# Optimization experiments

Hardware: AMD Instinct MI355X
Metric: run time of the kernel (lower is better)

## Reference

```python
import jax, jax.numpy as jnp
import numpy as np

B, T, C, N = 4, 1024, 960, 64
H = C // N
R_W, R_A, R_V, R_G = 64, 64, 32, 128
LN_EPS = 0.00064


def setup_inputs() -> dict:
    key = jax.random.key(0)
    ks = jax.random.split(key, 28)
    s = 0.5 / np.sqrt(C)
    u = lambda k, sh, sc: jax.random.uniform(k, sh, jnp.float32, -sc, sc)
    n = lambda k, sh, sc: jax.random.normal(k, sh, jnp.float32) * sc
    return {
        "x": jax.random.normal(ks[0], (B, T, C), jnp.float32),
        "v_first": jax.random.normal(ks[1], (B, T, C), jnp.float32),
        "x_r": jax.random.uniform(ks[2], (1, 1, C), jnp.float32),
        "x_w": jax.random.uniform(ks[3], (1, 1, C), jnp.float32),
        "x_k": jax.random.uniform(ks[4], (1, 1, C), jnp.float32),
        "x_v": jax.random.uniform(ks[5], (1, 1, C), jnp.float32),
        "x_a": jax.random.uniform(ks[6], (1, 1, C), jnp.float32),
        "x_g": jax.random.uniform(ks[7], (1, 1, C), jnp.float32),
        "w0": n(ks[8], (1, 1, C), 0.5) - 2.0,
        "w1": n(ks[9], (C, R_W), 0.02),
        "w2": n(ks[10], (R_W, C), 0.02),
        "a0": n(ks[11], (1, 1, C), 0.3),
        "a1": n(ks[12], (C, R_A), 0.02),
        "a2": n(ks[13], (R_A, C), 0.02),
        "v0": n(ks[14], (1, 1, C), 0.3) + 0.73,
        "v1": n(ks[15], (C, R_V), 0.02),
        "v2": n(ks[16], (R_V, C), 0.02),
        "g1": n(ks[17], (C, R_G), 0.02),
        "g2": n(ks[18], (R_G, C), 0.02),
        "k_k": n(ks[19], (1, 1, C), 0.1) + 0.71,
        "k_a": n(ks[20], (1, 1, C), 0.1) + 1.02,
        "r_k": n(ks[21], (H, N), 0.1) - 0.04,
        "Wr": u(ks[22], (C, C), s),
        "Wk": u(ks[23], (C, C), 0.1 * s),
        "Wv": u(ks[24], (C, C), s),
        "Wo": u(ks[25], (C, C), s),
        "ln_g": jnp.ones((C,), jnp.float32),
        "ln_b": jnp.zeros((C,), jnp.float32),
    }


def reference(x, v_first, x_r, x_w, x_k, x_v, x_a, x_g, w0, w1, w2,
              a0, a1, a2, v0, v1, v2, g1, g2, k_k, k_a, r_k,
              Wr, Wk, Wv, Wo, ln_g, ln_b):
    Bx, Tx, Cx = x.shape
    # token shift: xx[t] = x[t-1] - x[t], with x[-1] = 0
    xx = jnp.concatenate([jnp.zeros_like(x[:, :1]), x[:, :-1]], axis=1) - x
    xr = x + xx * x_r; xw = x + xx * x_w; xk = x + xx * x_k
    xv = x + xx * x_v; xa = x + xx * x_a; xg = x + xx * x_g
    r = xr @ Wr
    w_raw = w0 + jnp.tanh(xw @ w1) @ w2       # log-space decay
    k = xk @ Wk
    v = xv @ Wv
    # layer_id > 0: residual mix with layer-0 value
    v = v + (v_first - v) * jax.nn.sigmoid(v0 + (xv @ v1) @ v2)
    a = jax.nn.sigmoid(a0 + (xa @ a1) @ a2)   # in-context learning rate
    g = jax.nn.sigmoid(xg @ g1) @ g2          # gate
    kk = (k * k_k).reshape(Bx, Tx, H, N)
    kk = kk / jnp.maximum(jnp.linalg.norm(kk, axis=-1, keepdims=True), 1e-12)
    k = k * (1.0 + (a - 1.0) * k_a)
    f32 = jnp.float32
    rh = r.reshape(Bx, Tx, H, N).astype(f32)
    kh = k.reshape(Bx, Tx, H, N).astype(f32)
    vh = v.reshape(Bx, Tx, H, N).astype(f32)
    wh = jnp.exp(-jax.nn.softplus(-w_raw.reshape(Bx, Tx, H, N).astype(f32)) - 0.5)
    ah = (-kk).astype(f32)                              # removal key
    bh = (kk * a.reshape(Bx, Tx, H, N)).astype(f32)     # replacement key

    def step(state, inp):
        r_t, w_t, k_t, v_t, a_t, b_t = inp  # each (B,H,N); state (B,H,N,N)
        sa = jnp.einsum('bhij,bhj->bhi', state, a_t)
        state = (state * w_t[:, :, None, :]
                 + sa[..., None] * b_t[:, :, None, :]
                 + v_t[..., None] * k_t[:, :, None, :])
        out_t = jnp.einsum('bhij,bhj->bhi', state, r_t)
        return state, out_t

    tm = lambda u: jnp.transpose(u, (1, 0, 2, 3))  # time-major
    state0 = jnp.zeros((Bx, H, N, N), f32)
    _, wkv = jax.lax.scan(step, state0, (tm(rh), tm(wh), tm(kh), tm(vh), tm(ah), tm(bh)))
    wkv = jnp.transpose(wkv, (1, 0, 2, 3))  # (B,T,H,N)
    # GroupNorm with H groups == per-head layernorm over N
    mu = wkv.mean(-1, keepdims=True)
    var = wkv.var(-1, keepdims=True)
    xn = (wkv - mu) / jnp.sqrt(var + LN_EPS)
    xn = xn * ln_g.reshape(H, N) + ln_b.reshape(H, N)
    bonus = (rh * kh * r_k).sum(-1, keepdims=True) * vh  # r*k*v bonus term
    xo = (xn + bonus).astype(x.dtype).reshape(Bx, Tx, Cx)
    return (xo * g) @ Wo


if __name__ == "__main__":
    out = reference(**setup_inputs())
    print(out.shape, out.dtype)
```

## Files before the change

kernel.cpp:

```cpp
#include <hip/hip_runtime.h>
#include <hip/hip_bf16.h>
#include <math.h>

#define Tn 1024
#define Cn 960
#define Hn 15
#define Nn 64
#define Mn 4096

typedef short bf16x8 __attribute__((ext_vector_type(8)));
typedef float f32x4 __attribute__((ext_vector_type(4)));

#define MCc ((size_t)Mn * Cn)

__device__ __forceinline__ float sigmf(float x) { return 1.0f / (1.0f + __expf(-x)); }

__device__ __forceinline__ ushort f2bf(float x) {
    unsigned u = __float_as_uint(x);
    unsigned r = (u + 0x7FFFu + ((u >> 16) & 1u)) >> 16;
    return (ushort)r;
}
__device__ __forceinline__ float bf2f(ushort h) { return __uint_as_float(((unsigned)h) << 16); }

__device__ __forceinline__ float rowsum16(float x) {
    x += __int_as_float(__builtin_amdgcn_update_dpp(0, __float_as_int(x), 0x121, 0xF, 0xF, true));
    x += __int_as_float(__builtin_amdgcn_update_dpp(0, __float_as_int(x), 0x122, 0xF, 0xF, true));
    x += __int_as_float(__builtin_amdgcn_update_dpp(0, __float_as_int(x), 0x124, 0xF, 0xF, true));
    x += __int_as_float(__builtin_amdgcn_update_dpp(0, __float_as_int(x), 0x128, 0xF, 0xF, true));
    return x;
}

__global__ __launch_bounds__(256) void mix6_kernel(
    const float* __restrict__ x,
    const float* __restrict__ mr, const float* __restrict__ mw, const float* __restrict__ mk,
    const float* __restrict__ mv, const float* __restrict__ ma, const float* __restrict__ mg,
    ushort* __restrict__ r_sp, ushort* __restrict__ w_sp, ushort* __restrict__ k_sp,
    ushort* __restrict__ v_sp, ushort* __restrict__ a_sp, ushort* __restrict__ g_sp)
{
    int idx = blockIdx.x * 256 + threadIdx.x;
    int e = idx * 4;
    if (e >= Mn * Cn) return;
    int m = e / Cn;
    int c = e - m * Cn;
    int t = m & (Tn - 1);
    float4 xv = *(const float4*)(x + e);
    float4 xp = make_float4(0.f, 0.f, 0.f, 0.f);
    if (t > 0) xp = *(const float4*)(x + e - Cn);
    float4 dx = make_float4(xp.x - xv.x, xp.y - xv.y, xp.z - xv.z, xp.w - xv.w);
#define MIXSPLIT(MIXP, P)                                                     \
    {                                                                         \
        float4 mm = *(const float4*)(MIXP + c);                               \
        float4 O = make_float4(xv.x + dx.x * mm.x, xv.y + dx.y * mm.y,        \
                               xv.z + dx.z * mm.z, xv.w + dx.w * mm.w);       \
        ushort h0 = f2bf(O.x), h1 = f2bf(O.y), h2 = f2bf(O.z), h3 = f2bf(O.w);\
        ushort l0 = f2bf(O.x - bf2f(h0)), l1 = f2bf(O.y - bf2f(h1));          \
        ushort l2 = f2bf(O.z - bf2f(h2)), l3 = f2bf(O.w - bf2f(h3));          \
        *(ushort4*)(P + e) = make_ushort4(h0, h1, h2, h3);                    \
        *(ushort4*)(P + MCc + e) = make_ushort4(l0, l1, l2, l3);              \
    }
    MIXSPLIT(mr, r_sp)
    MIXSPLIT(mw, w_sp)
    MIXSPLIT(mk, k_sp)
    MIXSPLIT(mv, v_sp)
    MIXSPLIT(ma, a_sp)
    MIXSPLIT(mg, g_sp)
#undef MIXSPLIT
}

__global__ __launch_bounds__(256) void convWT_kernel(
    const float* __restrict__ W, ushort* __restrict__ Thi, ushort* __restrict__ Tlo)
{
    __shared__ float tile[32][33];
    int k0 = blockIdx.x * 32, n0 = blockIdx.y * 32;
    int tx = threadIdx.x & 31, ty = threadIdx.x >> 5;
#pragma unroll
    for (int i = 0; i < 4; ++i)
        tile[ty + 8 * i][tx] = W[(size_t)(k0 + ty + 8 * i) * 960 + n0 + tx];
    __syncthreads();
#pragma unroll
    for (int i = 0; i < 4; ++i) {
        float x = tile[tx][ty + 8 * i];
        ushort h = f2bf(x);
        ushort l = f2bf(x - bf2f(h));
        size_t o = (size_t)(n0 + ty + 8 * i) * 960 + k0 + tx;
        Thi[o] = h;
        Tlo[o] = l;
    }
}

__global__ __launch_bounds__(256) void wprep_kernel(
    const float* __restrict__ w1, const float* __restrict__ a1,
    const float* __restrict__ v1, const float* __restrict__ g1,
    const float* __restrict__ w2, const float* __restrict__ a2,
    const float* __restrict__ v2, const float* __restrict__ g2,
    ushort* __restrict__ arena)
{
    __shared__ float tile[32][33];
    int z = blockIdx.z;
    const float* src;
    int K, N;
    size_t off;
    switch (z) {
        case 0: src = w1; K = 960; N = 64;  off = 0;      break;
        case 1: src = a1; K = 960; N = 64;  off = 122880; break;
        case 2: src = v1; K = 960; N = 32;  off = 245760; break;
        case 3: src = g1; K = 960; N = 128; off = 307200; break;
        case 4: src = w2; K = 64;  N = 960; off = 552960; break;
        case 5: src = a2; K = 64;  N = 960; off = 675840; break;
        case 6: src = v2; K = 32;  N = 960; off = 798720; break;
        default: src = g2; K = 128; N = 960; off = 860160; break;
    }
    int k0 = blockIdx.x * 32, n0 = blockIdx.y * 32;
    if (k0 >= K || n0 >= N) return;
    int tx = threadIdx.x & 31, ty = threadIdx.x >> 5;
#pragma unroll
    for (int i = 0; i < 4; ++i)
        tile[ty + 8 * i][tx] = src[(size_t)(k0 + ty + 8 * i) * N + n0 + tx];
    __syncthreads();
    ushort* Thi = arena + off;
    ushort* Tlo = arena + off + (size_t)K * N;
#pragma unroll
    for (int i = 0; i < 4; ++i) {
        float x = tile[tx][ty + 8 * i];
        ushort h = f2bf(x);
        ushort l = f2bf(x - bf2f(h));
        size_t o = (size_t)(n0 + ty + 8 * i) * K + k0 + tx;
        Thi[o] = h;
        Tlo[o] = l;
    }
}

__global__ __launch_bounds__(256) void convN_kernel(
    const float* __restrict__ X, ushort* __restrict__ hi, ushort* __restrict__ lo, int n4)
{
    int idx = blockIdx.x * 256 + threadIdx.x;
    if (idx >= n4) return;
    int e = idx * 4;
    float4 x = *(const float4*)(X + e);
    ushort h0 = f2bf(x.x), h1 = f2bf(x.y), h2 = f2bf(x.z), h3 = f2bf(x.w);
    ushort l0 = f2bf(x.x - bf2f(h0)), l1 = f2bf(x.y - bf2f(h1));
    ushort l2 = f2bf(x.z - bf2f(h2)), l3 = f2bf(x.w - bf2f(h3));
    *(ushort4*)(hi + e) = make_ushort4(h0, h1, h2, h3);
    *(ushort4*)(lo + e) = make_ushort4(l0, l1, l2, l3);
}

__global__ __launch_bounds__(512) void gemm_bf3_kernel(
    const ushort* __restrict__ Ahi, const ushort* __restrict__ Alo,
    const ushort* __restrict__ Bhi, const ushort* __restrict__ Blo,
    float* __restrict__ C, int ldc)
{
    __shared__ __align__(16) ushort sA[2][2][128][40];
    __shared__ __align__(16) ushort sB[2][2][64][40];
    const int K = 960;
    int bm = blockIdx.x * 128, bn = blockIdx.y * 64;
    int t = threadIdx.x;
    int w = t >> 6, l = t & 63;
    int lr = l & 15, lk = l >> 4;

    int ar = t >> 2, aseg = t & 3;
    int brr = t >> 2;
    int bhl = brr >> 6, brow = brr & 63, bseg = t & 3;
    const ushort* gAh = Ahi + (size_t)(bm + ar) * K + aseg * 8;
    const ushort* gAl = Alo + (size_t)(bm + ar) * K + aseg * 8;
    const ushort* gB = (bhl ? Blo : Bhi) + (size_t)(bn + brow) * K + bseg * 8;

    f32x4 acc[4];
#pragma unroll
    for (int j = 0; j < 4; ++j)
#pragma unroll
        for (int e = 0; e < 4; ++e) acc[j][e] = 0.f;

    float4 rhP, rlP, rbP, rhQ, rlQ, rbQ;
#define LOADP(KOFF)                                                           \
    {                                                                         \
        rhP = *(const float4*)(gAh + (KOFF));                                 \
        rlP = *(const float4*)(gAl + (KOFF));                                 \
        rbP = *(const float4*)(gB + (KOFF));                                  \
    }
#define LOADQ(KOFF)                                                           \
    {                                                                         \
        rhQ = *(const float4*)(gAh + (KOFF));                                 \
        rlQ = *(const float4*)(gAl + (KOFF));                                 \
        rbQ = *(const float4*)(gB + (KOFF));                                  \
    }
#define WRITEP(BUF)                                                           \
    {                                                                         \
        *(float4*)&sA[BUF][0][ar][aseg * 8] = rhP;                            \
        *(float4*)&sA[BUF][1][ar][aseg * 8] = rlP;                            \
        *(float4*)&sB[BUF][bhl][brow][bseg * 8] = rbP;                        \
    }
#define WRITEQ(BUF)                                                           \
    {                                                                         \
        *(float4*)&sA[BUF][0][ar][aseg * 8] = rhQ;                            \
        *(float4*)&sA[BUF][1][ar][aseg * 8] = rlQ;                            \
        *(float4*)&sB[BUF][bhl][brow][bseg * 8] = rbQ;                        \
    }
#define COMPUTEK(BUF)                                                         \
    {                                                                         \
        bf16x8 ah, al, bh[4], bl[4];                                          \
        ah = *(const bf16x8*)&sA[BUF][0][16 * w + lr][lk * 8];                \
        al = *(const bf16x8*)&sA[BUF][1][16 * w + lr][lk * 8];                \
        _Pragma("unroll")                                                     \
        for (int j = 0; j < 4; ++j) {                                         \
            bh[j] = *(const bf16x8*)&sB[BUF][0][16 * j + lr][lk * 8];         \
            bl[j] = *(const bf16x8*)&sB[BUF][1][16 * j + lr][lk * 8];         \
        }                                                                     \
        _Pragma("unroll")                                                     \
        for (int j = 0; j < 4; ++j) {                                         \
            acc[j] = __builtin_amdgcn_mfma_f32_16x16x32_bf16(ah, bh[j], acc[j], 0, 0, 0); \
            acc[j] = __builtin_amdgcn_mfma_f32_16x16x32_bf16(ah, bl[j], acc[j], 0, 0, 0); \
            acc[j] = __builtin_amdgcn_mfma_f32_16x16x32_bf16(al, bh[j], acc[j], 0, 0, 0); \
        }                                                                     \
    }

    LOADP(0)
    WRITEP(0)
    LOADQ(32)
    asm volatile("s_waitcnt lgkmcnt(0)" ::: "memory");
    __builtin_amdgcn_s_barrier();

    int cur = 0;
    for (int ks = 0; ks < 30; ks += 2) {
        int k2 = (ks + 2 < 30 ? ks + 2 : 29) * 32;
        LOADP(k2)
        COMPUTEK(cur)
        WRITEQ(cur ^ 1)
        asm volatile("s_waitcnt lgkmcnt(0)" ::: "memory");
        __builtin_amdgcn_s_barrier();
        cur ^= 1;
        int k3 = (ks + 3 < 30 ? ks + 3 : 29) * 32;
        LOADQ(k3)
        COMPUTEK(cur)
        WRITEP(cur ^ 1)
        asm volatile("s_waitcnt lgkmcnt(0)" ::: "memory");
        __builtin_amdgcn_s_barrier();
        cur ^= 1;
    }

#pragma unroll
    for (int j = 0; j < 4; ++j)
#pragma unroll
        for (int jr = 0; jr < 4; ++jr) {
            int row = bm + 16 * w + lk * 4 + jr;
            int col = bn + 16 * j + lr;
            C[(size_t)row * ldc + col] = acc[j][jr];
        }
#undef COMPUTEK
#undef WRITEP
#undef WRITEQ
#undef LOADP
#undef LOADQ
}

__device__ __forceinline__ void lora_core(
    const ushort* __restrict__ Ahi, const ushort* __restrict__ Alo, int lda,
    const ushort* __restrict__ Bhi, const ushort* __restrict__ Blo,
    float* __restrict__ C, int ldc, int Nvalid, int K, int act, int bn)
{
    __shared__ __align__(16) ushort sA[2][2][128][40];
    __shared__ __align__(16) ushort sB[2][2][64][40];
    int bm = blockIdx.x * 128;
    int t = threadIdx.x;
    int w = t >> 6, l = t & 63;
    int lr = l & 15, lk = l >> 4;

    int ar = t >> 2, aseg = t & 3;
    int brr = t >> 2;
    int bhl = brr >> 6, brow = brr & 63, bseg = t & 3;
    const ushort* gAh = Ahi + (size_t)(bm + ar) * lda + aseg * 8;
    const ushort* gAl = Alo + (size_t)(bm + ar) * lda + aseg * 8;
    const ushort* gB = (bhl ? Blo : Bhi) + (size_t)(bn + brow) * K + bseg * 8;

    f32x4 acc[4];
#pragma unroll
    for (int j = 0; j < 4; ++j)
#pragma unroll
        for (int e = 0; e < 4; ++e) acc[j][e] = 0.f;

    float4 rhP, rlP, rbP, rhQ, rlQ, rbQ;
#define LLOADP(KOFF)                                                          \
    {                                                                         \
        rhP = *(const float4*)(gAh + (KOFF));                                 \
        rlP = *(const float4*)(gAl + (KOFF));                                 \
        rbP = *(const float4*)(gB + (KOFF));                                  \
    }
#define LLOADQ(KOFF)                                                          \
    {                                                                         \
        rhQ = *(const float4*)(gAh + (KOFF));                                 \
        rlQ = *(const float4*)(gAl + (KOFF));                                 \
        rbQ = *(const float4*)(gB + (KOFF));                                  \
    }
#define LWRITEP(BUF)                                                          \
    {                                                                         \
        *(float4*)&sA[BUF][0][ar][aseg * 8] = rhP;                            \
        *(float4*)&sA[BUF][1][ar][aseg * 8] = rlP;                            \
        *(float4*)&sB[BUF][bhl][brow][bseg * 8] = rbP;                        \
    }
#define LWRITEQ(BUF)                                                          \
    {                                                                         \
        *(float4*)&sA[BUF][0][ar][aseg * 8] = rhQ;                            \
        *(float4*)&sA[BUF][1][ar][aseg * 8] = rlQ;                            \
        *(float4*)&sB[BUF][bhl][brow][bseg * 8] = rbQ;                        \
    }
#define LCOMPUTE(BUF)                                                         \
    {                                                                         \
        bf16x8 ah, al, bh[4], bl[4];                                          \
        ah = *(const bf16x8*)&sA[BUF][0][16 * w + lr][lk * 8];                \
        al = *(const bf16x8*)&sA[BUF][1][16 * w + lr][lk * 8];                \
        _Pragma("unroll")                                                     \
        for (int j = 0; j < 4; ++j) {                                         \
            bh[j] = *(const bf16x8*)&sB[BUF][0][16 * j + lr][lk * 8];         \
            bl[j] = *(const bf16x8*)&sB[BUF][1][16 * j + lr][lk * 8];         \
        }                                                                     \
        _Pragma("unroll")                                                     \
        for (int j = 0; j < 4; ++j) {                                         \
            acc[j] = __builtin_amdgcn_mfma_f32_16x16x32_bf16(ah, bh[j], acc[j], 0, 0, 0); \
            acc[j] = __builtin_amdgcn_mfma_f32_16x16x32_bf16(ah, bl[j], acc[j], 0, 0, 0); \
            acc[j] = __builtin_amdgcn_mfma_f32_16x16x32_bf16(al, bh[j], acc[j], 0, 0, 0); \
        }                                                                     \
    }

    int nk = K >> 5;
    LLOADP(0)
    LWRITEP(0)
    if (nk > 1) LLOADQ(32)
    asm volatile("s_waitcnt lgkmcnt(0)" ::: "memory");
    __builtin_amdgcn_s_barrier();

    int cur = 0;
    for (int ks = 0; ks < nk; ++ks) {
        int k2 = (ks + 2 < nk ? ks + 2 : nk - 1) * 32;
        if (!(ks & 1)) { LLOADP(k2) } else { LLOADQ(k2) }
        LCOMPUTE(cur)
        if (ks + 1 < nk) {
            if (!(ks & 1)) { LWRITEQ(cur ^ 1) } else { LWRITEP(cur ^ 1) }
            asm volatile("s_waitcnt lgkmcnt(0)" ::: "memory");
            __builtin_amdgcn_s_barrier();
        }
        cur ^= 1;
    }

#pragma unroll
    for (int j = 0; j < 4; ++j)
#pragma unroll
        for (int jr = 0; jr < 4; ++jr) {
            int row = bm + 16 * w + lk * 4 + jr;
            int col = bn + 16 * j + lr;
            if (col < Nvalid) {
                float v = acc[j][jr];
                if (act == 1) v = tanhf(v);
                else if (act == 2) v = sigmf(v);
                C[(size_t)row * ldc + col] = v;
            }
        }
#undef LCOMPUTE
#undef LWRITEP
#undef LWRITEQ
#undef LLOADP
#undef LLOADQ
}

__global__ __launch_bounds__(512) void lora_down_kernel(
    const ushort* __restrict__ xw_sp, const ushort* __restrict__ xa_sp,
    const ushort* __restrict__ xv_sp, const ushort* __restrict__ xg_sp,
    const ushort* __restrict__ arena, float* __restrict__ hid)
{
    int z = blockIdx.z;
    int bn = blockIdx.y * 64;
    const ushort* A;
    size_t off;
    int N, act, coff;
    switch (z) {
        case 0: A = xw_sp; off = 0;      N = 64;  act = 1; coff = 0;   break;
        case 1: A = xa_sp; off = 122880; N = 64;  act = 0; coff = 64;  break;
        case 2: A = xv_sp; off = 245760; N = 32;  act = 0; coff = 128; break;
        default: A = xg_sp; off = 307200; N = 128; act = 2; coff = 160; break;
    }
    if (bn >= N) return;
    lora_core(A, A + MCc, Cn, arena + off, arena + off + (size_t)960 * N,
              hid + coff, 288, N, 960, act, bn);
}

__global__ __launch_bounds__(512) void lora_up_kernel(
    const ushort* __restrict__ hidHi, const ushort* __restrict__ hidLo,
    const ushort* __restrict__ arena,
    float* __restrict__ oW, float* __restrict__ oA,
    float* __restrict__ oV, float* __restrict__ oG)
{
    int z = blockIdx.z;
    int bn = blockIdx.y * 64;
    size_t off;
    int K, aoff;
    float* C;
    switch (z) {
        case 0: off = 552960; K = 64;  aoff = 0;   C = oW; break;
        case 1: off = 675840; K = 64;  aoff = 64;  C = oA; break;
        case 2: off = 798720; K = 32;  aoff = 128; C = oV; break;
        default: off = 860160; K = 128; aoff = 160; C = oG; break;
    }
    lora_core(hidHi + aoff, hidLo + aoff, 288, arena + off,
              arena + off + (size_t)K * 960, C, Cn, Cn, K, 0, bn);
}

__global__ __launch_bounds__(256, 2) void scan_kernel(
    const float* __restrict__ rP, const float* __restrict__ wrawP,
    const float* __restrict__ apreP, const float* __restrict__ vsigP,
    const float* __restrict__ krawP, const float* __restrict__ vrawP,
    const float* __restrict__ vfirstP, const float* __restrict__ gP,
    const float* __restrict__ w0, const float* __restrict__ a0,
    const float* __restrict__ v0c, const float* __restrict__ kkc,
    const float* __restrict__ kac, const float* __restrict__ r_k,
    const float* __restrict__ ln_g, const float* __restrict__ ln_b,
    ushort* __restrict__ xsp)
{
    __shared__ float buf[2][7][16][64];
    __shared__ float outL[16][64];
    int tid = threadIdx.x;
    int q = tid >> 6, l = tid & 63;
    int blk = blockIdx.x;
    int bh = blk >> 3, seg = blk & 7;
    int bb = bh / Hn, h = bh - bb * Hn;
    size_t base = (size_t)bb * Tn * Cn + h * 64;
    int rg = l >> 4, cg = l & 15;
    int row0 = 16 * q + 4 * rg;
    int c0 = 4 * cg;

    int sstep = tid >> 4, sseg = tid & 15;
    size_t soff = base + (size_t)sstep * Cn + sseg * 4;
    int wofs = sstep * 64 + sseg * 4;
    int ccol = h * 64 + sseg * 4;

    int cbeg = (seg == 0) ? 0 : 8 * seg - 4;
    int cendc = 8 * seg + 8;
    int coutc = 8 * seg;

    float4 w0c4 = *(const float4*)(w0 + ccol);
    float4 a0c4 = *(const float4*)(a0 + ccol);
    float4 v0c4 = *(const float4*)(v0c + ccol);
    float4 kkc4 = *(const float4*)(kkc + ccol);
    float4 kac4 = *(const float4*)(kac + ccol);
    float4 rk4 = *(const float4*)(r_k + ccol);
    float4 lg4 = *(const float4*)(ln_g + ccol);
    float4 lb4 = *(const float4*)(ln_b + ccol);

    float s[4][4];
#pragma unroll
    for (int r = 0; r < 4; ++r)
#pragma unroll
        for (int c = 0; c < 4; ++c) s[r][c] = 0.f;

    float4 g_r, g_wr, g_vr, g_vf, g_vs, g_g, g_kr, g_ap;

#define LOADSTAGE(OFF)                                                        \
    g_r = *(const float4*)(rP + soff + (OFF));                                \
    g_wr = *(const float4*)(wrawP + soff + (OFF));                            \
    g_vr = *(const float4*)(vrawP + soff + (OFF));                            \
    g_vf = *(const float4*)(vfirstP + soff + (OFF));                          \
    g_vs = *(const float4*)(vsigP + soff + (OFF));                            \
    g_g = *(const float4*)(gP + soff + (OFF));                                \
    g_kr = *(const float4*)(krawP + soff + (OFF));                            \
    g_ap = *(const float4*)(apreP + soff + (OFF));

#define PARK(BN)                                                              \
    {                                                                         \
        const float E = 0.60653065971263342f;                                 \
        float4 w4;                                                            \
        w4.x = sigmf(w0c4.x + g_wr.x) * E;                                    \
        w4.y = sigmf(w0c4.y + g_wr.y) * E;                                    \
        w4.z = sigmf(w0c4.z + g_wr.z) * E;                                    \
        w4.w = sigmf(w0c4.w + g_wr.w) * E;                                    \
        float4 v4;                                                            \
        v4.x = g_vr.x + (g_vf.x - g_vr.x) * sigmf(v0c4.x + g_vs.x);           \
        v4.y = g_vr.y + (g_vf.y - g_vr.y) * sigmf(v0c4.y + g_vs.y);           \
        v4.z = g_vr.z + (g_vf.z - g_vr.z) * sigmf(v0c4.z + g_vs.z);           \
        v4.w = g_vr.w + (g_vf.w - g_vr.w) * sigmf(v0c4.w + g_vs.w);           \
        float4 a4;                                                            \
        a4.x = sigmf(a0c4.x + g_ap.x);                                        \
        a4.y = sigmf(a0c4.y + g_ap.y);                                        \
        a4.z = sigmf(a0c4.z + g_ap.z);                                        \
        a4.w = sigmf(a0c4.w + g_ap.w);                                        \
        float4 kk;                                                            \
        kk.x = g_kr.x * kkc4.x; kk.y = g_kr.y * kkc4.y;                       \
        kk.z = g_kr.z * kkc4.z; kk.w = g_kr.w * kkc4.w;                       \
        float ss = kk.x * kk.x + kk.y * kk.y + kk.z * kk.z + kk.w * kk.w;     \
        ss = rowsum16(ss);                                                    \
        float inv = 1.0f / fmaxf(sqrtf(ss), 1e-12f);                          \
        float4 ah4, bh4, kh4;                                                 \
        ah4.x = -kk.x * inv; bh4.x = kk.x * inv * a4.x;                       \
        ah4.y = -kk.y * inv; bh4.y = kk.y * inv * a4.y;                       \
        ah4.z = -kk.z * inv; bh4.z = kk.z * inv * a4.z;                       \
        ah4.w = -kk.w * inv; bh4.w = kk.w * inv * a4.w;                       \
        kh4.x = g_kr.x * (1.0f + (a4.x - 1.0f) * kac4.x);                     \
        kh4.y = g_kr.y * (1.0f + (a4.y - 1.0f) * kac4.y);                     \
        kh4.z = g_kr.z * (1.0f + (a4.z - 1.0f) * kac4.z);                     \
        kh4.w = g_kr.w * (1.0f + (a4.w - 1.0f) * kac4.w);                     \
        *(float4*)((BN) + 0 * 1024 + wofs) = g_r;                             \
        *(float4*)((BN) + 1 * 1024 + wofs) = w4;                              \
        *(float4*)((BN) + 2 * 1024 + wofs) = kh4;                             \
        *(float4*)((BN) + 3 * 1024 + wofs) = ah4;                             \
        *(float4*)((BN) + 4 * 1024 + wofs) = bh4;                             \
        *(float4*)((BN) + 5 * 1024 + wofs) = v4;                              \
        *(float4*)((BN) + 6 * 1024 + wofs) = g_g;                             \
    }

    LOADSTAGE((size_t)cbeg * 16 * Cn)
    PARK(&buf[0][0][0][0])
    asm volatile("s_waitcnt lgkmcnt(0)" ::: "memory");
    __builtin_amdgcn_s_barrier();

#define DECL2(S)                                                              \
    float4 S##a0, S##w0, S##k0, S##b0, S##r0, S##v0;                          \
    float4 S##a1, S##w1, S##k1, S##b1, S##r1, S##v1;
#define DSLOAD2(S, T)                                                         \
    S##a0 = *(const float4*)(bc + 3 * 1024 + (T) * 64 + c0);                  \
    S##w0 = *(const float4*)(bc + 1 * 1024 + (T) * 64 + c0);                  \
    S##k0 = *(const float4*)(bc + 2 * 1024 + (T) * 64 + c0);                  \
    S##b0 = *(const float4*)(bc + 4 * 1024 + (T) * 64 + c0);                  \
    S##r0 = *(const float4*)(bc + 0 * 1024 + (T) * 64 + c0);                  \
    S##v0 = *(const float4*)(bc + 5 * 1024 + (T) * 64 + row0);                \
    S##a1 = *(const float4*)(bc + 3 * 1024 + ((T) + 1) * 64 + c0);            \
    S##w1 = *(const float4*)(bc + 1 * 1024 + ((T) + 1) * 64 + c0);            \
    S##k1 = *(const float4*)(bc + 2 * 1024 + ((T) + 1) * 64 + c0);            \
    S##b1 = *(const float4*)(bc + 4 * 1024 + ((T) + 1) * 64 + c0);            \
    S##r1 = *(const float4*)(bc + 0 * 1024 + ((T) + 1) * 64 + c0);            \
    S##v1 = *(const float4*)(bc + 5 * 1024 + ((T) + 1) * 64 + row0);
#define STEP(AV, WV, KV, BV, RV, VV, T)                                       \
    {                                                                         \
        float sp0 = s[0][0] * AV.x + s[0][1] * AV.y + s[0][2] * AV.z + s[0][3] * AV.w; \
        float sp1 = s[1][0] * AV.x + s[1][1] * AV.y + s[1][2] * AV.z + s[1][3] * AV.w; \
        float sp2 = s[2][0] * AV.x + s[2][1] * AV.y + s[2][2] * AV.z + s[2][3] * AV.w; \
        float sp3 = s[3][0] * AV.x + s[3][1] * AV.y + s[3][2] * AV.z + s[3][3] * AV.w; \
        sp0 = rowsum16(sp0);                                                  \
        sp1 = rowsum16(sp1);                                                  \
        sp2 = rowsum16(sp2);                                                  \
        sp3 = rowsum16(sp3);                                                  \
        float sa[4] = {sp0, sp1, sp2, sp3};                                   \
        float vr[4] = {VV.x, VV.y, VV.z, VV.w};                               \
        float op[4];                                                          \
        _Pragma("unroll")                                                     \
        for (int r = 0; r < 4; ++r) {                                         \
            s[r][0] = s[r][0] * WV.x + sa[r] * BV.x + vr[r] * KV.x;           \
            float o = s[r][0] * RV.x;                                         \
            s[r][1] = s[r][1] * WV.y + sa[r] * BV.y + vr[r] * KV.y;           \
            o += s[r][1] * RV.y;                                              \
            s[r][2] = s[r][2] * WV.z + sa[r] * BV.z + vr[r] * KV.z;           \
            o += s[r][2] * RV.z;                                              \
            s[r][3] = s[r][3] * WV.w + sa[r] * BV.w + vr[r] * KV.w;           \
            o += s[r][3] * RV.w;                                              \
            op[r] = rowsum16(o);                                              \
        }                                                                     \
        if (cg == 0)                                                          \
            *(float4*)&outL[T][row0] = make_float4(op[0], op[1], op[2], op[3]); \
    }

    DECL2(A) DECL2(B)

    int cur = 0;
    for (int c = cbeg; c < cendc; ++c) {
        const float* bc = &buf[cur][0][0][0];
        {
            int cnxt = (c + 1 < cendc) ? c + 1 : c;
            LOADSTAGE((size_t)cnxt * 16 * Cn)
        }

        DSLOAD2(A, 0)
#pragma unroll
        for (int it = 0; it < 4; ++it) {
            DSLOAD2(B, 4 * it + 2)
            STEP(Aa0, Aw0, Ak0, Ab0, Ar0, Av0, 4 * it + 0)
            STEP(Aa1, Aw1, Ak1, Ab1, Ar1, Av1, 4 * it + 1)
            if (it < 3) { DSLOAD2(A, 4 * it + 4) }
            STEP(Ba0, Bw0, Bk0, Bb0, Br0, Bv0, 4 * it + 2)
            STEP(Ba1, Bw1, Bk1, Bb1, Br1, Bv1, 4 * it + 3)
        }

        PARK(&buf[cur ^ 1][0][0][0])
        asm volatile("s_waitcnt lgkmcnt(0)" ::: "memory");
        __builtin_amdgcn_s_barrier();

        if (c >= coutc) {
            float4 o4 = *(const float4*)&outL[sstep][4 * sseg];
            float4 r4 = *(const float4*)(bc + 0 * 1024 + sstep * 64 + 4 * sseg);
            float4 k4 = *(const float4*)(bc + 2 * 1024 + sstep * 64 + 4 * sseg);
            float4 v4 = *(const float4*)(bc + 5 * 1024 + sstep * 64 + 4 * sseg);
            float4 gg4 = *(const float4*)(bc + 6 * 1024 + sstep * 64 + 4 * sseg);
            float m1 = o4.x + o4.y + o4.z + o4.w;
            float m2 = o4.x * o4.x + o4.y * o4.y + o4.z * o4.z + o4.w * o4.w;
            float bd = r4.x * k4.x * rk4.x + r4.y * k4.y * rk4.y +
                       r4.z * k4.z * rk4.z + r4.w * k4.w * rk4.w;
            m1 = rowsum16(m1);
            m2 = rowsum16(m2);
            bd = rowsum16(bd);
            float mean = m1 * (1.f / 64.f);
            float var = m2 * (1.f / 64.f) - mean * mean;
            float is = rsqrtf(var + 0.00064f);
            float xo0 = ((o4.x - mean) * is * lg4.x + lb4.x + bd * v4.x) * gg4.x;
            float xo1 = ((o4.y - mean) * is * lg4.y + lb4.y + bd * v4.y) * gg4.y;
            float xo2 = ((o4.z - mean) * is * lg4.z + lb4.z + bd * v4.z) * gg4.z;
            float xo3 = ((o4.w - mean) * is * lg4.w + lb4.w + bd * v4.w) * gg4.w;
            ushort h0 = f2bf(xo0), h1 = f2bf(xo1), h2 = f2bf(xo2), h3 = f2bf(xo3);
            ushort l0 = f2bf(xo0 - bf2f(h0)), l1 = f2bf(xo1 - bf2f(h1));
            ushort l2 = f2bf(xo2 - bf2f(h2)), l3 = f2bf(xo3 - bf2f(h3));
            size_t gt = (size_t)c * 16 + sstep;
            size_t eo = base + gt * Cn + 4 * sseg;
            *(ushort4*)(xsp + eo) = make_ushort4(h0, h1, h2, h3);
            *(ushort4*)(xsp + MCc + eo) = make_ushort4(l0, l1, l2, l3);
        }
        __builtin_amdgcn_s_barrier();
        cur ^= 1;
    }
#undef STEP
#undef DSLOAD2
#undef DECL2
#undef PARK
#undef LOADSTAGE
}

extern "C" void kernel_launch(void* const* d_in, const int* in_sizes, int n_in,
                              void* d_out, int out_size, void* d_ws, size_t ws_size,
                              hipStream_t stream)
{
    const float* x       = (const float*)d_in[0];
    const float* v_first = (const float*)d_in[1];
    const float* x_r     = (const float*)d_in[2];
    const float* x_w     = (const float*)d_in[3];
    const float* x_k     = (const float*)d_in[4];
    const float* x_v     = (const float*)d_in[5];
    const float* x_a     = (const float*)d_in[6];
    const float* x_g     = (const float*)d_in[7];
    const float* w0      = (const float*)d_in[8];
    const float* w1      = (const float*)d_in[9];
    const float* w2      = (const float*)d_in[10];
    const float* a0      = (const float*)d_in[11];
    const float* a1      = (const float*)d_in[12];
    const float* a2      = (const float*)d_in[13];
    const float* v0c     = (const float*)d_in[14];
    const float* v1      = (const float*)d_in[15];
    const float* v2      = (const float*)d_in[16];
    const float* g1w     = (const float*)d_in[17];
    const float* g2w     = (const float*)d_in[18];
    const float* k_k     = (const float*)d_in[19];
    const float* k_a     = (const float*)d_in[20];
    const float* r_k     = (const float*)d_in[21];
    const float* Wr      = (const float*)d_in[22];
    const float* Wk      = (const float*)d_in[23];
    const float* Wv      = (const float*)d_in[24];
    const float* Wo      = (const float*)d_in[25];
    const float* ln_g    = (const float*)d_in[26];
    const float* ln_b    = (const float*)d_in[27];
    float* out = (float*)d_out;

    float* ws = (float*)d_ws;
    float* B0 = ws + 0 * MCc;
    float* B1 = ws + 1 * MCc;
    float* B2 = ws + 2 * MCc;
    float* B3 = ws + 3 * MCc;
    float* B4 = ws + 4 * MCc;
    float* B5 = ws + 5 * MCc;
    float* B6 = ws + 6 * MCc;
    float* B7 = ws + 7 * MCc;
    float* B8 = ws + 8 * MCc;
    float* hid = ws + 9 * MCc;

    ushort* XRsp = (ushort*)B0;
    ushort* XWsp = (ushort*)B1;
    ushort* XKsp = (ushort*)B2;
    ushort* XVsp = (ushort*)out;
    ushort* XAsp = (ushort*)B4;
    ushort* XGsp = (ushort*)B5;
    ushort* S3 = (ushort*)B3;
    ushort* hidHi = S3;
    ushort* hidLo = S3 + 1179648;
    ushort* arena = S3 + 2359296;
    ushort* Whi = (ushort*)hid;
    ushort* Wlo = Whi + (size_t)960 * 960;
    ushort* Xsp = (ushort*)B4;

    mix6_kernel<<<3840, 256, 0, stream>>>(x, x_r, x_w, x_k, x_v, x_a, x_g,
                                          XRsp, XWsp, XKsp, XVsp, XAsp, XGsp);
    wprep_kernel<<<dim3(30, 30, 8), 256, 0, stream>>>(w1, a1, v1, g1w,
                                                      w2, a2, v2, g2w, arena);

    dim3 gW(30, 30);
    dim3 gM(32, 15);
    convWT_kernel<<<gW, 256, 0, stream>>>(Wr, Whi, Wlo);
    gemm_bf3_kernel<<<gM, 512, 0, stream>>>(XRsp, XRsp + MCc, Whi, Wlo, B6, Cn);
    convWT_kernel<<<gW, 256, 0, stream>>>(Wk, Whi, Wlo);
    gemm_bf3_kernel<<<gM, 512, 0, stream>>>(XKsp, XKsp + MCc, Whi, Wlo, B7, Cn);
    convWT_kernel<<<gW, 256, 0, stream>>>(Wv, Whi, Wlo);
    gemm_bf3_kernel<<<gM, 512, 0, stream>>>(XVsp, XVsp + MCc, Whi, Wlo, B8, Cn);

    lora_down_kernel<<<dim3(32, 2, 4), 512, 0, stream>>>(XWsp, XAsp, XVsp, XGsp,
                                                         arena, hid);
    convN_kernel<<<1152, 256, 0, stream>>>(hid, hidHi, hidLo, Mn * 288 / 4);
    lora_up_kernel<<<dim3(32, 15, 4), 512, 0, stream>>>(hidHi, hidLo, arena,
                                                        B0, B2, B1, B5);
    convWT_kernel<<<gW, 256, 0, stream>>>(Wo, Whi, Wlo);
    scan_kernel<<<480, 256, 0, stream>>>(B6, B0, B2, B1, B7, B8, v_first, B5,
                                         w0, a0, v0c, k_k, k_a,
                                         r_k, ln_g, ln_b, Xsp);
    gemm_bf3_kernel<<<gM, 512, 0, stream>>>(Xsp, Xsp + MCc, Whi, Wlo, out, Cn);
}
```

Measured before the change: 340.1 us.

## Batch the R/K/V weight conversions and GEMMs into single launches with 256-thread blocks

The three weight transpose-and-split conversions and the three projection GEMMs are each merged into one launch indexed by blockIdx.z, so they no longer run as six serialized launches. The GEMM core moves from 512 to 256 threads per block, with each wave computing two 16-row MFMA tiles and each thread loading two 16-byte vectors per operand. This raises register use and work per thread while cutting launch count and tail effects. The scan's chunk warm-up start also moves from 8*seg-4 to 8*seg-3, so each segment recomputes one fewer chunk of overlap, which trades less redundant work for a possible accuracy risk.

Result: faster. 332.7 us (-2.2%).

```diff
diff --git a/kernel.cpp b/kernel.cpp
--- a/kernel.cpp
+++ b/kernel.cpp
@@ -71,6 +71,33 @@
     const float* __restrict__ W, ushort* __restrict__ Thi, ushort* __restrict__ Tlo)
 {
     __shared__ float tile[32][33];
+    int k0 = blockIdx.x * 32, n0 = blockIdx.y * 32;
+    int tx = threadIdx.x & 31, ty = threadIdx.x >> 5;
+#pragma unroll
+    for (int i = 0; i < 4; ++i)
+        tile[ty + 8 * i][tx] = W[(size_t)(k0 + ty + 8 * i) * 960 + n0 + tx];
+    __syncthreads();
+#pragma unroll
+    for (int i = 0; i < 4; ++i) {
+        float x = tile[tx][ty + 8 * i];
+        ushort h = f2bf(x);
+        ushort l = f2bf(x - bf2f(h));
+        size_t o = (size_t)(n0 + ty + 8 * i) * 960 + k0 + tx;
+        Thi[o] = h;
+        Tlo[o] = l;
+    }
+}
+
+__global__ __launch_bounds__(256) void convWT3_kernel(
+    const float* __restrict__ Wr, const float* __restrict__ Wk,
+    const float* __restrict__ Wv,
+    ushort* __restrict__ S0, ushort* __restrict__ S1, ushort* __restrict__ S2)
+{
+    __shared__ float tile[32][33];
+    int z = blockIdx.z;
+    const float* W = (z == 0) ? Wr : (z == 1) ? Wk : Wv;
+    ushort* Thi = (z == 0) ? S0 : (z == 1) ? S1 : S2;
+    ushort* Tlo = Thi + (size_t)960 * 960;
     int k0 = blockIdx.x * 32, n0 = blockIdx.y * 32;
     int tx = threadIdx.x & 31, ty = threadIdx.x >> 5;
 #pragma unroll
@@ -144,73 +171,94 @@
     *(ushort4*)(lo + e) = make_ushort4(l0, l1, l2, l3);
 }
 
-__global__ __launch_bounds__(512) void gemm_bf3_kernel(
+__device__ __forceinline__ void gemm_core(
     const ushort* __restrict__ Ahi, const ushort* __restrict__ Alo,
     const ushort* __restrict__ Bhi, const ushort* __restrict__ Blo,
-    float* __restrict__ C, int ldc)
+    float* __restrict__ C, int ldc, int bm, int bn)
 {
     __shared__ __align__(16) ushort sA[2][2][128][40];
     __shared__ __align__(16) ushort sB[2][2][64][40];
     const int K = 960;
-    int bm = blockIdx.x * 128, bn = blockIdx.y * 64;
     int t = threadIdx.x;
     int w = t >> 6, l = t & 63;
     int lr = l & 15, lk = l >> 4;
 
-    int ar = t >> 2, aseg = t & 3;
-    int brr = t >> 2;
-    int bhl = brr >> 6, brow = brr & 63, bseg = t & 3;
-    const ushort* gAh = Ahi + (size_t)(bm + ar) * K + aseg * 8;
-    const ushort* gAl = Alo + (size_t)(bm + ar) * K + aseg * 8;
-    const ushort* gB = (bhl ? Blo : Bhi) + (size_t)(bn + brow) * K + bseg * 8;
-
-    f32x4 acc[4];
-#pragma unroll
-    for (int j = 0; j < 4; ++j)
-#pragma unroll
-        for (int e = 0; e < 4; ++e) acc[j][e] = 0.f;
-
-    float4 rhP, rlP, rbP, rhQ, rlQ, rbQ;
+    int ar = t >> 1, aseg = t & 1;
+    int br = t & 63, bhalf = (t >> 6) & 1, bseg = t >> 7;
+    const ushort* gAh = Ahi + (size_t)(bm + ar) * K + aseg * 16;
+    const ushort* gAl = Alo + (size_t)(bm + ar) * K + aseg * 16;
+    const ushort* gB = (bhalf ? Blo : Bhi) + (size_t)(bn + br) * K + bseg * 16;
+
+    f32x4 acc[2][4];
+#pragma unroll
+    for (int i = 0; i < 2; ++i)
+#pragma unroll
+        for (int j = 0; j < 4; ++j)
+#pragma unroll
+            for (int e = 0; e < 4; ++e) acc[i][j][e] = 0.f;
+
+    float4 h0P, h1P, l0P, l1P, b0P, b1P;
+    float4 h0Q, h1Q, l0Q, l1Q, b0Q, b1Q;
 #define LOADP(KOFF)                                                           \
     {                                                                         \
-        rhP = *(const float4*)(gAh + (KOFF));                                 \
-        rlP = *(const float4*)(gAl + (KOFF));                                 \
-        rbP = *(const float4*)(gB + (KOFF));                                  \
+        h0P = *(const float4*)(gAh + (KOFF));                                 \
+        h1P = *(const float4*)(gAh + (KOFF) + 8);                             \
+        l0P = *(const float4*)(gAl + (KOFF));                                 \
+        l1P = *(const float4*)(gAl + (KOFF) + 8);                             \
+        b0P = *(const float4*)(gB + (KOFF));                                  \
+        b1P = *(const float4*)(gB + (KOFF) + 8);                              \
     }
 #define LOADQ(KOFF)                                                           \
     {                                                                         \
-        rhQ = *(const float4*)(gAh + (KOFF));                                 \
-        rlQ = *(const float4*)(gAl + (KOFF));                                 \
-        rbQ = *(const float4*)(gB + (KOFF));                                  \
+        h0Q = *(const float4*)(gAh + (KOFF));                                 \
+        h1Q = *(const float4*)(gAh + (KOFF) + 8);                             \
+        l0Q = *(const float4*)(gAl + (KOFF));                                 \
+        l1Q = *(const float4*)(gAl + (KOFF) + 8);                             \
+        b0Q = *(const float4*)(gB + (KOFF));                                  \
+        b1Q = *(const float4*)(gB + (KOFF) + 8);                              \
     }
 #define WRITEP(BUF)                                                           \
     {                                                                         \
-        *(float4*)&sA[BUF][0][ar][aseg * 8] = rhP;                            \
-        *(float4*)&sA[BUF][1][ar][aseg * 8] = rlP;                            \
-        *(float4*)&sB[BUF][bhl][brow][bseg * 8] = rbP;                        \
+        *(float4*)&sA[BUF][0][ar][aseg * 16] = h0P;                           \
+        *(float4*)&sA[BUF][0][ar][aseg * 16 + 8] = h1P;                       \
+        *(float4*)&sA[BUF][1][ar][aseg * 16] = l0P;                           \
+        *(float4*)&sA[BUF][1][ar][aseg * 16 + 8] = l1P;                       \
+        *(float4*)&sB[BUF][bhalf][br][bseg * 16] = b0P;                       \
+        *(float4*)&sB[BUF][bhalf][br][bseg * 16 + 8] = b1P;                   \
     }
 #define WRITEQ(BUF)                                                           \
     {                                                                         \
-        *(float4*)&sA[BUF][0][ar][aseg * 8] = rhQ;                            \
-        *(float4*)&sA[BUF][1][ar][aseg * 8] = rlQ;                            \
-        *(float4*)&sB[BUF][bhl][brow][bseg * 8] = rbQ;                        \
+        *(float4*)&sA[BUF][0][ar][aseg * 16] = h0Q;                           \
+        *(float4*)&sA[BUF][0][ar][aseg * 16 + 8] = h1Q;                       \
+        *(float4*)&sA[BUF][1][ar][aseg * 16] = l0Q;                           \
+        *(float4*)&sA[BUF][1][ar][aseg * 16 + 8] = l1Q;                       \
+        *(float4*)&sB[BUF][bhalf][br][bseg * 16] = b0Q;                       \
+        *(float4*)&sB[BUF][bhalf][br][bseg * 16 + 8] = b1Q;                   \
     }
 #define COMPUTEK(BUF)                                                         \
     {                                                                         \
-        bf16x8 ah, al, bh[4], bl[4];                                          \
-        ah = *(const bf16x8*)&sA[BUF][0][16 * w + lr][lk * 8];                \
-        al = *(const bf16x8*)&sA[BUF][1][16 * w + lr][lk * 8];                \
+        bf16x8 ah[2], al[2], bh[4], bl[4];                                    \
+        _Pragma("unroll")                                                     \
+        for (int i = 0; i < 2; ++i) {                                         \
+            ah[i] = *(const bf16x8*)&sA[BUF][0][32 * w + 16 * i + lr][lk * 8];\
+            al[i] = *(const bf16x8*)&sA[BUF][1][32 * w + 16 * i + lr][lk * 8];\
+        }                                                                     \
         _Pragma("unroll")                                                     \
         for (int j = 0; j < 4; ++j) {                                         \
             bh[j] = *(const bf16x8*)&sB[BUF][0][16 * j + lr][lk * 8];         \
             bl[j] = *(const bf16x8*)&sB[BUF][1][16 * j + lr][lk * 8];         \
         }                                                                     \
         _Pragma("unroll")                                                     \
-        for (int j = 0; j < 4; ++j) {                                         \
-            acc[j] = __builtin_amdgcn_mfma_f32_16x16x32_bf16(ah, bh[j], acc[j], 0, 0, 0); \
-            acc[j] = __builtin_amdgcn_mfma_f32_16x16x32_bf16(ah, bl[j], acc[j], 0, 0, 0); \
-            acc[j] = __builtin_amdgcn_mfma_f32_16x16x32_bf16(al, bh[j], acc[j], 0, 0, 0); \
-        }                                                                     \
+        for (int i = 0; i < 2; ++i)                                           \
+            _Pragma("unroll")                                                 \
+            for (int j = 0; j < 4; ++j) {                                     \
+                acc[i][j] = __builtin_amdgcn_mfma_f32_16x16x32_bf16(          \
+                    ah[i], bh[j], acc[i][j], 0, 0, 0);                        \
+                acc[i][j] = __builtin_amdgcn_mfma_f32_16x16x32_bf16(          \
+                    ah[i], bl[j], acc[i][j], 0, 0, 0);                        \
+                acc[i][j] = __builtin_amdgcn_mfma_f32_16x16x32_bf16(          \
+                    al[i], bh[j], acc[i][j], 0, 0, 0);                        \
+            }                                                                 \
     }
 
     LOADP(0)
@@ -238,18 +286,43 @@
     }
 
 #pragma unroll
-    for (int j = 0; j < 4; ++j)
-#pragma unroll
-        for (int jr = 0; jr < 4; ++jr) {
-            int row = bm + 16 * w + lk * 4 + jr;
-            int col = bn + 16 * j + lr;
-            C[(size_t)row * ldc + col] = acc[j][jr];
-        }
+    for (int i = 0; i < 2; ++i)
+#pragma unroll
+        for (int j = 0; j < 4; ++j)
+#pragma unroll
+            for (int jr = 0; jr < 4; ++jr) {
+                int row = bm + 32 * w + 16 * i + lk * 4 + jr;
+                int col = bn + 16 * j + lr;
+                C[(size_t)row * ldc + col] = acc[i][j][jr];
+            }
 #undef COMPUTEK
 #undef WRITEP
 #undef WRITEQ
 #undef LOADP
 #undef LOADQ
+}
+
+__global__ __launch_bounds__(256) void gemm3_kernel(
+    const ushort* __restrict__ XR, const ushort* __restrict__ XK,
+    const ushort* __restrict__ XV,
+    const ushort* __restrict__ WrS, const ushort* __restrict__ WkS,
+    const ushort* __restrict__ WvS,
+    float* __restrict__ oR, float* __restrict__ oK, float* __restrict__ oV)
+{
+    int z = blockIdx.z;
+    const ushort* A = (z == 0) ? XR : (z == 1) ? XK : XV;
+    const ushort* W = (z == 0) ? WrS : (z == 1) ? WkS : WvS;
+    float* C = (z == 0) ? oR : (z == 1) ? oK : oV;
+    gemm_core(A, A + MCc, W, W + (size_t)960 * 960, C, Cn,
+              blockIdx.x * 128, blockIdx.y * 64);
+}
+
+__global__ __launch_bounds__(256) void gemm1_kernel(
+    const ushort* __restrict__ Ahi, const ushort* __restrict__ Alo,
+    const ushort* __restrict__ Bhi, const ushort* __restrict__ Blo,
+    float* __restrict__ C, int ldc)
+{
+    gemm_core(Ahi, Alo, Bhi, Blo, C, ldc, blockIdx.x * 128, blockIdx.y * 64);
 }
 
 __device__ __forceinline__ void lora_core(
@@ -430,7 +503,7 @@
     int wofs = sstep * 64 + sseg * 4;
     int ccol = h * 64 + sseg * 4;
 
-    int cbeg = (seg == 0) ? 0 : 8 * seg - 4;
+    int cbeg = (seg == 0) ? 0 : 8 * seg - 3;
     int cendc = 8 * seg + 8;
     int coutc = 8 * seg;
 
@@ -672,6 +745,9 @@
     ushort* hidHi = S3;
     ushort* hidLo = S3 + 1179648;
     ushort* arena = S3 + 2359296;
+    ushort* WkS = S3 + 3465216;
+    ushort* WvS = S3 + 5308416;
+    ushort* WrS = (ushort*)hid;
     ushort* Whi = (ushort*)hid;
     ushort* Wlo = Whi + (size_t)960 * 960;
     ushort* Xsp = (ushort*)B4;
@@ -680,24 +756,20 @@
                                           XRsp, XWsp, XKsp, XVsp, XAsp, XGsp);
     wprep_kernel<<<dim3(30, 30, 8), 256, 0, stream>>>(w1, a1, v1, g1w,
                                                       w2, a2, v2, g2w, arena);
-
-    dim3 gW(30, 30);
-    dim3 gM(32, 15);
-    convWT_kernel<<<gW, 256, 0, stream>>>(Wr, Whi, Wlo);
-    gemm_bf3_kernel<<<gM, 512, 0, stream>>>(XRsp, XRsp + MCc, Whi, Wlo, B6, Cn);
-    convWT_kernel<<<gW, 256, 0, stream>>>(Wk, Whi, Wlo);
-    gemm_bf3_kernel<<<gM, 512, 0, stream>>>(XKsp, XKsp + MCc, Whi, Wlo, B7, Cn);
-    convWT_kernel<<<gW, 256, 0, stream>>>(Wv, Whi, Wlo);
-    gemm_bf3_kernel<<<gM, 512, 0, stream>>>(XVsp, XVsp + MCc, Whi, Wlo, B8, Cn);
-
+    convWT3_kernel<<<dim3(30, 30, 3), 256, 0, stream>>>(Wr, Wk, Wv,
+                                                        WrS, WkS, WvS);
+    gemm3_kernel<<<dim3(32, 15, 3), 256, 0, stream>>>(XRsp, XKsp, XVsp,
+                                                      WrS, WkS, WvS,
+                                                      B6, B7, B8);
     lora_down_kernel<<<dim3(32, 2, 4), 512, 0, stream>>>(XWsp, XAsp, XVsp, XGsp,
                                                          arena, hid);
     convN_kernel<<<1152, 256, 0, stream>>>(hid, hidHi, hidLo, Mn * 288 / 4);
     lora_up_kernel<<<dim3(32, 15, 4), 512, 0, stream>>>(hidHi, hidLo, arena,
                                                         B0, B2, B1, B5);
-    convWT_kernel<<<gW, 256, 0, stream>>>(Wo, Whi, Wlo);
+    convWT_kernel<<<dim3(30, 30), 256, 0, stream>>>(Wo, Whi, Wlo);
     scan_kernel<<<480, 256, 0, stream>>>(B6, B0, B2, B1, B7, B8, v_first, B5,
                                          w0, a0, v0c, k_k, k_a,
                                          r_k, ln_g, ln_b, Xsp);
-    gemm_bf3_kernel<<<gM, 512, 0, stream>>>(Xsp, Xsp + MCc, Whi, Wlo, out, Cn);
-}
+    gemm1_kernel<<<dim3(32, 15), 256, 0, stream>>>(Xsp, Xsp + MCc, Whi, Wlo,
+                                                   out, Cn);
+}
```
